# Performance work log

Measured on AMD Instinct MI355X. Metric: run time of the kernel, lower is better.

The kernel has to match this reference:

```python
import jax, jax.numpy as jnp
import numpy as np

B, D_IN = 8192, 4096
H1, H2, LAT = 2048, 1024, 256
NQ, NL = 16, 2


def setup_inputs() -> dict:
    key = jax.random.key(0)
    ks = jax.random.split(key, 16)
    def lin(k, fan_in, fan_out):
        k1, k2 = jax.random.split(k)
        s = 1.0 / np.sqrt(fan_in)
        W = jax.random.uniform(k1, (fan_out, fan_in), jnp.float32, -s, s)
        b = jax.random.uniform(k2, (fan_out,), jnp.float32, -s, s)
        return W, b
    x = jax.random.normal(ks[0], (B, D_IN), jnp.float32)
    We1, be1 = lin(ks[1], D_IN, H1)
    We2, be2 = lin(ks[2], H1, H2)
    We3, be3 = lin(ks[3], H2, LAT)
    P = jax.random.normal(ks[4], (NL, NQ, 3), jnp.float32)  # ansatz params (rx,ry,rz)
    Wd1, bd1 = lin(ks[5], NQ, H2)
    Wd2, bd2 = lin(ks[6], H2, H1)
    Wd3, bd3 = lin(ks[7], H1, D_IN)
    return {"x": x, "We1": We1, "be1": be1, "We2": We2, "be2": be2,
            "We3": We3, "be3": be3, "P": P, "Wd1": Wd1, "bd1": bd1,
            "Wd2": Wd2, "bd2": bd2, "Wd3": Wd3, "bd3": bd3}


def _quantum_block(latent, P):
    """Exact simulation of the per-qubit circuit (all gates single-qubit, so the
    2^n statevector factorizes into per-qubit 2-vectors (a,b) over |0>,|1>).
    latent: (B, LAT), P: (NL, NQ, 3). Returns Z-expectations (B, NQ)."""
    nq = P.shape[1]
    th = latent[:, :nq]  # encoding RY angles, (B, NQ)
    # RY(th)|0> = cos(th/2)|0> + sin(th/2)|1>
    a = jnp.cos(th / 2).astype(jnp.complex64)  # (B, NQ)
    b = jnp.sin(th / 2).astype(jnp.complex64)
    for l in range(P.shape[0]):
        # RX
        t = P[l, :, 0] / 2
        c, s = jnp.cos(t).astype(jnp.complex64), jnp.sin(t).astype(jnp.complex64)
        a, b = c * a - 1j * s * b, -1j * s * a + c * b
        # RY
        t = P[l, :, 1] / 2
        c, s = jnp.cos(t).astype(jnp.complex64), jnp.sin(t).astype(jnp.complex64)
        a, b = c * a - s * b, s * a + c * b
        # RZ
        t = P[l, :, 2] / 2
        ph = jnp.exp(-1j * t.astype(jnp.complex64))
        a, b = a * ph, b * jnp.conj(ph)
    z = (a.real ** 2 + a.imag ** 2) - (b.real ** 2 + b.imag ** 2)
    return z.astype(latent.dtype)


def reference(x, We1, be1, We2, be2, We3, be3, P,
              Wd1, bd1, Wd2, bd2, Wd3, bd3):
    h = jax.nn.relu(x @ We1.T + be1)
    h = jax.nn.relu(h @ We2.T + be2)
    latent = h @ We3.T + be3            # (B, LAT)
    refined = _quantum_block(latent, P)  # (B, NQ)
    h = jax.nn.relu(refined @ Wd1.T + bd1)
    h = jax.nn.relu(h @ Wd2.T + bd2)
    return h @ Wd3.T + bd3              # (B, D_IN)
```

## Files before the change

kernel.cpp:

```cpp
#include <hip/hip_runtime.h>

typedef __attribute__((ext_vector_type(8))) short bf16x8;
typedef __attribute__((ext_vector_type(16))) float f32x16;

__device__ __forceinline__ unsigned short f2bf(float f) {
    union { float f; unsigned int u; } v; v.f = f;
    unsigned int u = v.u;
    unsigned int r = (u + 0x7FFFu + ((u >> 16) & 1u)) >> 16;
    return (unsigned short)r;
}
__device__ __forceinline__ float bf2f(unsigned short b) {
    union { unsigned int u; float f; } v; v.u = ((unsigned int)b) << 16;
    return v.f;
}

#define GL16(g, l)                                                             \
    __builtin_amdgcn_global_load_lds(                                          \
        (__attribute__((address_space(1))) void*)(void*)(g),                   \
        (__attribute__((address_space(3))) void*)(void*)(l), 16, 0, 0)

#define BAR()   __builtin_amdgcn_s_barrier()
#define LGKM0() asm volatile("s_waitcnt lgkmcnt(0)" ::: "memory")

struct Cast5 {
    const float *s0, *s1, *s2, *s3, *s4;
    unsigned short *d0, *d1, *d2, *d3, *d4;
    int n0, n1, n2, n3, total;
};
__global__ void castall(Cast5 a) {
    int stride = gridDim.x * blockDim.x;
    for (int i = blockIdx.x * blockDim.x + threadIdx.x; i < a.total; i += stride) {
        int j = i; const float* s; unsigned short* d;
        if (j < a.n0) { s = a.s0; d = a.d0; }
        else { j -= a.n0;
            if (j < a.n1) { s = a.s1; d = a.d1; }
            else { j -= a.n1;
                if (j < a.n2) { s = a.s2; d = a.d2; }
                else { j -= a.n2;
                    if (j < a.n3) { s = a.s3; d = a.d3; }
                    else { j -= a.n3; s = a.s4; d = a.d4; } } } }
        float4 v = ((const float4*)s)[j];
        ushort4 o;
        o.x = f2bf(v.x); o.y = f2bf(v.y); o.z = f2bf(v.z); o.w = f2bf(v.w);
        ((ushort4*)d)[j] = o;
    }
}


template<int RELU, int OUT_BF16, int MP>
__global__ __launch_bounds__(512, 2) void gemm8p(
    const unsigned short* __restrict__ A,
    const unsigned short* __restrict__ Bm,
    const float* __restrict__ bias,
    void* __restrict__ Cout,
    int N, int K, int NT)
{
    constexpr int RT   = MP / 2;
    constexpr int AHU  = MP * 2048;
    constexpr int BOFF = MP * 8192;
    __shared__ __align__(16) unsigned short lds[MP * 8192 + 32768];

    const int tid  = threadIdx.x;
    const int lane = tid & 63;
    const int w    = tid >> 6;
    const int wm   = w >> 2;
    const int wn   = w & 3;
    const int bm   = blockIdx.y;
    const int bn   = blockIdx.x;

    const unsigned short* gA = A  + (long)bm * (MP * 64) * K;
    const unsigned short* gB = Bm + (long)bn * 256 * K;

    const int sr0 = tid >> 3;
    const int so0 = (((tid & 7) * 16) ^ ((sr0 & 7) << 4)) >> 1;
    const int loff = (sr0 * K + so0) * 2;
    const int ch1  = K * 128;
    const int lb0 = (w * 64) * 8;
    const int lb1 = (512 + w * 64) * 8;

    const int l31  = lane & 31;
    const int hi16 = (lane >> 5) * 16;
    const int aRow = wm * (MP * 16) + l31;
    const int bRow = wn * 32 + l31;
    const int swA  = (aRow & 7) << 4;
    const int swB  = (bRow & 7) << 4;
    int aK[4], bK[4];
    #pragma unroll
    for (int ks = 0; ks < 4; ++ks) {
        aK[ks] = aRow * 128 + ((ks * 32 + hi16) ^ swA);
        bK[ks] = MP * 16384 + bRow * 128 + ((ks * 32 + hi16) ^ swB);
    }

    f32x16 acc[2][2][RT] = {};
    bf16x8 a0[RT][4], a1[RT][4], b0[4], b1[4];

#define GLA_(SP, DI) do {                                                      \
        GL16((const char*)(SP) + loff, &lds[0] + (DI) + lb0);                  \
        if constexpr (MP == 4) {                                               \
            GL16((const char*)(SP) + loff + ch1, &lds[0] + (DI) + lb1); }      \
    } while (0)
#define GLB_(SP, DI) do {                                                      \
        GL16((const char*)(SP) + loff, &lds[0] + (DI) + lb0);                  \
        GL16((const char*)(SP) + loff + ch1, &lds[0] + (DI) + lb1);            \
    } while (0)

#define READA_(AR, MH, PAR) do {                                               \
        _Pragma("unroll") for (int rt_ = 0; rt_ < RT; ++rt_)                   \
        _Pragma("unroll") for (int ks_ = 0; ks_ < 4; ++ks_)                    \
            AR[rt_][ks_] = *(const bf16x8*)((const char*)lds + aK[ks_] +       \
                           (((PAR)*2+(MH))*MP*4096 + rt_*4096));               \
    } while (0)
#define READB_(BR, NH, PAR) do {                                               \
        _Pragma("unroll") for (int ks_ = 0; ks_ < 4; ++ks_)                    \
            BR[ks_] = *(const bf16x8*)((const char*)lds + bK[ks_] +            \
                      (((PAR)*2+(NH))*16384));                                 \
    } while (0)
#define QUAD(mh, nh, AR, BR) do {                                              \
        __builtin_amdgcn_s_setprio(1);                                         \
        _Pragma("unroll") for (int ks_ = 0; ks_ < 4; ++ks_)                    \
        _Pragma("unroll") for (int rt_ = 0; rt_ < RT; ++rt_)                   \
            acc[mh][nh][rt_] = __builtin_amdgcn_mfma_f32_32x32x16_bf16(        \
                AR[rt_][ks_], BR[ks_], acc[mh][nh][rt_], 0, 0, 0);             \
        __builtin_amdgcn_s_setprio(0);                                         \
    } while (0)
#define VMW() do {                                                             \
        if constexpr (MP == 4) asm volatile("s_waitcnt vmcnt(6)" ::: "memory");\
        else                   asm volatile("s_waitcnt vmcnt(5)" ::: "memory");\
    } while (0)

    GLB_(gB,                      BOFF + 0);
    GLA_(gA,                      0);
    GLB_(gB + (long)128 * K,      BOFF + 8192);
    GLA_(gA + (long)(MP*32) * K,  AHU);
    GLB_(gB + 64,                 BOFF + 2*8192);
    GLA_(gA + 64,                 2*AHU);
    GLB_(gB + (long)128 * K + 64, BOFF + 3*8192);
    VMW();
    BAR();
    READA_(a0, 0, 0);
    READB_(b0, 0, 0);

    const unsigned short* sA1 = gA + (long)(MP*32) * K + 64;
    const unsigned short* sA0 = gA + 128;
    const unsigned short* sB0 = gB + 128;
    const unsigned short* sB1 = gB + (long)128 * K + 128;

#define KTILE(T, PAR) do {                                                     \
        const int adv1_ = ((T) + 2 < NT) ? 64 : 0;                             \
        const int adv2_ = ((T) + 3 < NT) ? 64 : 0;                             \
                                                                       \
        READA_(a1, 1, PAR);                                                    \
        GLA_(sA1, (((PAR)^1)*2+1)*AHU); sA1 += adv1_;                          \
        BAR();                                                                 \
        QUAD(0, 0, a0, b0);                                                    \
                                                                       \
        READB_(b1, 1, PAR);                                                    \
        GLB_(sB0, BOFF + (PAR)*2*8192); sB0 += adv2_;                          \
        VMW();                                                                 \
        BAR();                                                                 \
        QUAD(0, 1, a0, b1);                                                    \
                                                                       \
        READA_(a0, 0, (PAR)^1);                                                \
        GLA_(sA0, (PAR)*2*AHU); sA0 += adv2_;                                  \
        BAR();                                                                 \
        QUAD(1, 1, a1, b1);                                                    \
                                                                       \
        GLB_(sB1, BOFF + ((PAR)*2+1)*8192); sB1 += adv2_;                      \
        VMW();                                                                 \
        BAR();                                                                 \
        QUAD(1, 0, a1, b0);                                                    \
        READB_(b0, 0, (PAR)^1);                                                \
    } while (0)

    for (int t = 0; t < NT; t += 2) {
        KTILE(t, 0);
        KTILE(t + 1, 1);
    }

    asm volatile("s_waitcnt vmcnt(0)" ::: "memory");
    BAR();

    const int rbase = (lane >> 5) * 4;
    float bv[2];
    #pragma unroll
    for (int nh = 0; nh < 2; ++nh)
        bv[nh] = bias[(long)bn * 256 + nh * 128 + wn * 32 + l31];

    if (OUT_BF16) {
        unsigned short* epi = lds;
        #pragma unroll
        for (int h = 0; h < 2; ++h) {
            if (h) { LGKM0(); BAR(); }
            #pragma unroll
            for (int rt = 0; rt < RT; ++rt)
                #pragma unroll
                for (int nh = 0; nh < 2; ++nh) {
                    int lcol = nh * 128 + wn * 32 + l31;
                    #pragma unroll
                    for (int reg = 0; reg < 16; ++reg) {
                        float v = acc[h][nh][rt][reg] + bv[nh];
                        if (RELU) v = fmaxf(v, 0.f);
                        int lrow = wm * (MP * 16) + rt * 32 +
                                   (reg & 3) + ((reg >> 2) << 3) + rbase;
                        epi[lrow * 264 + lcol] = f2bf(v);
                    }
                }
            LGKM0();
            BAR();
            long rowg0 = (long)bm * (MP * 64) + h * (MP * 32);
            #pragma unroll
            for (int i = 0; i < 2 * MP; ++i) {
                int row = (tid >> 5) + i * 16;
                int cc  = (tid & 31) * 8;
                bf16x8 v8 = *(const bf16x8*)&epi[row * 264 + cc];
                *(bf16x8*)((unsigned short*)Cout + (rowg0 + row) * (long)N + (long)bn * 256 + cc) = v8;
            }
        }
    } else {
        #pragma unroll
        for (int mh = 0; mh < 2; ++mh)
            #pragma unroll
            for (int rt = 0; rt < RT; ++rt)
                #pragma unroll
                for (int nh = 0; nh < 2; ++nh) {
                    long gcol = (long)bn * 256 + nh * 128 + wn * 32 + l31;
                    long growb = (long)bm * (MP * 64) + mh * (MP * 32) +
                                 wm * (MP * 16) + rt * 32 + rbase;
                    #pragma unroll
                    for (int reg = 0; reg < 16; ++reg) {
                        float v = acc[mh][nh][rt][reg] + bv[nh];
                        if (RELU) v = fmaxf(v, 0.f);
                        long grow = growb + (reg & 3) + ((reg >> 2) << 3);
                        ((float*)Cout)[grow * (long)N + gcol] = v;
                    }
                }
    }
#undef GLA_
#undef GLB_
#undef READA_
#undef READB_
#undef QUAD
#undef VMW
#undef KTILE
}

__global__ __launch_bounds__(256) void latq_d1(
    const unsigned short* __restrict__ h2,
    const float* __restrict__ We3,
    const float* __restrict__ be3,
    const float* __restrict__ P,
    const float* __restrict__ Wd1,
    const float* __restrict__ bd1,
    unsigned short* __restrict__ h3)
{
    __shared__ float zsh[4][16];
    const int lane = threadIdx.x & 63;
    const int wv   = threadIdx.x >> 6;
    const long row = (long)blockIdx.x * 4 + wv;

    float hreg[16];
    const unsigned short* hr = h2 + row * 1024;
    #pragma unroll
    for (int j = 0; j < 16; ++j) hreg[j] = bf2f(hr[lane + 64 * j]);

    float myth = 0.f;
    #pragma unroll
    for (int q = 0; q < 16; ++q) {
        const float* wq = We3 + q * 1024;
        float p = 0.f;
        #pragma unroll
        for (int j = 0; j < 16; ++j) p += hreg[j] * wq[lane + 64 * j];
        #pragma unroll
        for (int o = 32; o; o >>= 1) p += __shfl_xor(p, o, 64);
        if (lane == q) myth = p + be3[q];
    }

    if (lane < 16) {
        const int q = lane;
        float ar = cosf(0.5f * myth), ai = 0.f;
        float br = sinf(0.5f * myth), bi = 0.f;
        #pragma unroll
        for (int l = 0; l < 2; ++l) {
            const float* pp = P + (l * 16 + q) * 3;
            float t, c, s, ar2, ai2, br2, bi2;
            t = 0.5f * pp[0]; c = cosf(t); s = sinf(t);
            ar2 = c * ar + s * bi;  ai2 = c * ai - s * br;
            br2 = c * br + s * ai;  bi2 = c * bi - s * ar;
            ar = ar2; ai = ai2; br = br2; bi = bi2;
            t = 0.5f * pp[1]; c = cosf(t); s = sinf(t);
            ar2 = c * ar - s * br;  ai2 = c * ai - s * bi;
            br2 = s * ar + c * br;  bi2 = s * ai + c * bi;
            ar = ar2; ai = ai2; br = br2; bi = bi2;
            t = 0.5f * pp[2]; c = cosf(t); s = sinf(t);
            ar2 = ar * c + ai * s;  ai2 = ai * c - ar * s;
            br2 = br * c - bi * s;  bi2 = bi * c + br * s;
            ar = ar2; ai = ai2; br = br2; bi = bi2;
        }
        zsh[wv][q] = ar * ar + ai * ai - (br * br + bi * bi);
    }
    __syncthreads();

    float z[16];
    #pragma unroll
    for (int q = 0; q < 16; ++q) z[q] = zsh[wv][q];

    unsigned short* orow = h3 + row * 1024;
    #pragma unroll
    for (int i = 0; i < 16; ++i) {
        int j = lane + 64 * i;
        const float4* wrow = (const float4*)(Wd1 + j * 16);
        float acc = bd1[j];
        #pragma unroll
        for (int qq = 0; qq < 4; ++qq) {
            float4 w4 = wrow[qq];
            acc += z[qq * 4 + 0] * w4.x + z[qq * 4 + 1] * w4.y
                 + z[qq * 4 + 2] * w4.z + z[qq * 4 + 3] * w4.w;
        }
        orow[j] = f2bf(fmaxf(acc, 0.f));
    }
}

extern "C" void kernel_launch(void* const* d_in, const int* in_sizes, int n_in,
                              void* d_out, int out_size, void* d_ws, size_t ws_size,
                              hipStream_t stream) {
    const float* x   = (const float*)d_in[0];
    const float* We1 = (const float*)d_in[1];
    const float* be1 = (const float*)d_in[2];
    const float* We2 = (const float*)d_in[3];
    const float* be2 = (const float*)d_in[4];
    const float* We3 = (const float*)d_in[5];
    const float* be3 = (const float*)d_in[6];
    const float* P   = (const float*)d_in[7];
    const float* Wd1 = (const float*)d_in[8];
    const float* bd1 = (const float*)d_in[9];
    const float* Wd2 = (const float*)d_in[10];
    const float* bd2 = (const float*)d_in[11];
    const float* Wd3 = (const float*)d_in[12];
    const float* bd3 = (const float*)d_in[13];

    const int B = 8192, DIN = 4096, NH1 = 2048, NH2 = 1024;

    char* w = (char*)d_ws;
    unsigned short* x_bf   = (unsigned short*)(w);
    unsigned short* h4     = x_bf;
    unsigned short* We1_bf = (unsigned short*)(w + 67108864L);
    unsigned short* We2_bf = (unsigned short*)(w + 83886080L);
    unsigned short* Wd2_bf = (unsigned short*)(w + 88080384L);
    unsigned short* Wd3_bf = (unsigned short*)(w + 92274688L);
    unsigned short* h1     = (unsigned short*)(w + 109051904L);
    unsigned short* h3     = h1;
    unsigned short* h2     = (unsigned short*)(w + 142606336L);

    Cast5 ca;
    ca.s0 = x;   ca.d0 = x_bf;   ca.n0 = (int)((long)B * DIN / 4);
    ca.s1 = We1; ca.d1 = We1_bf; ca.n1 = (int)((long)NH1 * DIN / 4);
    ca.s2 = We2; ca.d2 = We2_bf; ca.n2 = (int)((long)NH2 * NH1 / 4);
    ca.s3 = Wd2; ca.d3 = Wd2_bf; ca.n3 = (int)((long)NH1 * NH2 / 4);
    ca.s4 = Wd3; ca.d4 = Wd3_bf;
    ca.total = ca.n0 + ca.n1 + ca.n2 + ca.n3 + (int)((long)DIN * NH1 / 4);
    castall<<<2048, 256, 0, stream>>>(ca);

    gemm8p<1, 1, 4><<<dim3(NH1 / 256, B / 256), 512, 0, stream>>>(x_bf, We1_bf, be1, h1, NH1, DIN, DIN >> 6);
    gemm8p<1, 1, 2><<<dim3(NH2 / 256, B / 128), 512, 0, stream>>>(h1, We2_bf, be2, h2, NH2, NH1, NH1 >> 6);
    latq_d1<<<dim3(B / 4), 256, 0, stream>>>(h2, We3, be3, P, Wd1, bd1, h3);
    gemm8p<1, 1, 4><<<dim3(NH1 / 256, B / 256), 512, 0, stream>>>(h3, Wd2_bf, bd2, h4, NH1, NH2, NH2 >> 6);
    gemm8p<0, 0, 4><<<dim3(DIN / 256, B / 256), 512, 0, stream>>>(h4, Wd3_bf, bd3, d_out, DIN, NH1, NH1 >> 6);
}
```

Measured before the change: 440.2 us.

## Switch GEMM LDS tile layout from XOR-swizzled rows to k-chunk-major columns

Changes how A and B tiles are laid out in LDS. Global loads now map consecutive threads to consecutive rows of one 16-byte k-chunk, so each chunk lands contiguously in LDS instead of in XOR-swizzled 128-byte rows. MFMA operand reads then use simple linear offsets with no per-lane swizzle. The aim is to cut LDS bank conflicts and address arithmetic on the reads, at the cost of less coalesced global loads, since each thread now fetches 16 bytes from a different row.

```diff
diff --git a/kernel.cpp b/kernel.cpp
--- a/kernel.cpp
+++ b/kernel.cpp
@@ -56,9 +56,12 @@
     int N, int K, int NT)
 {
     constexpr int RT   = MP / 2;
-    constexpr int AHU  = MP * 2048;
-    constexpr int BOFF = MP * 8192;
+    constexpr int ARWS = MP * 32;
+    constexpr int ASH  = (MP == 4) ? 7 : 6;
+    constexpr int AHB  = MP * 4096;
+    constexpr int BOFFB = 4 * AHB;
     __shared__ __align__(16) unsigned short lds[MP * 8192 + 32768];
+    char* ldsc = (char*)lds;
 
     const int tid  = threadIdx.x;
     const int lane = tid & 63;
@@ -71,49 +74,38 @@
     const unsigned short* gA = A  + (long)bm * (MP * 64) * K;
     const unsigned short* gB = Bm + (long)bn * 256 * K;
 
-    const int sr0 = tid >> 3;
-    const int so0 = (((tid & 7) * 16) ^ ((sr0 & 7) << 4)) >> 1;
-    const int loff = (sr0 * K + so0) * 2;
-    const int ch1  = K * 128;
-    const int lb0 = (w * 64) * 8;
-    const int lb1 = (512 + w * 64) * 8;
+    const int loffA = (tid & (ARWS - 1)) * (K * 2) + (tid >> ASH) * 16;
+    const int loffB = (tid & 127) * (K * 2) + (tid >> 7) * 16;
+    const int lwb   = w * 1024;
 
     const int l31  = lane & 31;
-    const int hi16 = (lane >> 5) * 16;
-    const int aRow = wm * (MP * 16) + l31;
-    const int bRow = wn * 32 + l31;
-    const int swA  = (aRow & 7) << 4;
-    const int swB  = (bRow & 7) << 4;
-    int aK[4], bK[4];
-    #pragma unroll
-    for (int ks = 0; ks < 4; ++ks) {
-        aK[ks] = aRow * 128 + ((ks * 32 + hi16) ^ swA);
-        bK[ks] = MP * 16384 + bRow * 128 + ((ks * 32 + hi16) ^ swB);
-    }
+    const int hi   = lane >> 5;
+    const int aBase = wm * (MP * 256) + l31 * 16 + hi * (ARWS * 16);
+    const int bBase = BOFFB + wn * 512 + l31 * 16 + hi * 2048;
 
     f32x16 acc[2][2][RT] = {};
     bf16x8 a0[RT][4], a1[RT][4], b0[4], b1[4];
 
 #define GLA_(SP, DI) do {                                                      \
-        GL16((const char*)(SP) + loff, &lds[0] + (DI) + lb0);                  \
+        GL16((const char*)(SP) + loffA, ldsc + (DI) + lwb);                    \
         if constexpr (MP == 4) {                                               \
-            GL16((const char*)(SP) + loff + ch1, &lds[0] + (DI) + lb1); }      \
+            GL16((const char*)(SP) + loffA + 64, ldsc + (DI) + 8192 + lwb); }  \
     } while (0)
 #define GLB_(SP, DI) do {                                                      \
-        GL16((const char*)(SP) + loff, &lds[0] + (DI) + lb0);                  \
-        GL16((const char*)(SP) + loff + ch1, &lds[0] + (DI) + lb1);            \
+        GL16((const char*)(SP) + loffB, ldsc + (DI) + lwb);                    \
+        GL16((const char*)(SP) + loffB + 64, ldsc + (DI) + 8192 + lwb);        \
     } while (0)
 
 #define READA_(AR, MH, PAR) do {                                               \
         _Pragma("unroll") for (int rt_ = 0; rt_ < RT; ++rt_)                   \
         _Pragma("unroll") for (int ks_ = 0; ks_ < 4; ++ks_)                    \
-            AR[rt_][ks_] = *(const bf16x8*)((const char*)lds + aK[ks_] +       \
-                           (((PAR)*2+(MH))*MP*4096 + rt_*4096));               \
+            AR[rt_][ks_] = *(const bf16x8*)(ldsc + aBase +                     \
+                (((PAR)*2+(MH))*AHB + rt_*512 + ks_*(ARWS*32)));               \
     } while (0)
 #define READB_(BR, NH, PAR) do {                                               \
         _Pragma("unroll") for (int ks_ = 0; ks_ < 4; ++ks_)                    \
-            BR[ks_] = *(const bf16x8*)((const char*)lds + bK[ks_] +            \
-                      (((PAR)*2+(NH))*16384));                                 \
+            BR[ks_] = *(const bf16x8*)(ldsc + bBase +                          \
+                (((PAR)*2+(NH))*16384 + ks_*4096));                            \
     } while (0)
 #define QUAD(mh, nh, AR, BR) do {                                              \
         __builtin_amdgcn_s_setprio(1);                                         \
@@ -128,13 +120,13 @@
         else                   asm volatile("s_waitcnt vmcnt(5)" ::: "memory");\
     } while (0)
 
-    GLB_(gB,                      BOFF + 0);
+    GLB_(gB,                      BOFFB + 0);
     GLA_(gA,                      0);
-    GLB_(gB + (long)128 * K,      BOFF + 8192);
-    GLA_(gA + (long)(MP*32) * K,  AHU);
-    GLB_(gB + 64,                 BOFF + 2*8192);
-    GLA_(gA + 64,                 2*AHU);
-    GLB_(gB + (long)128 * K + 64, BOFF + 3*8192);
+    GLB_(gB + (long)128 * K,      BOFFB + 16384);
+    GLA_(gA + (long)(MP*32) * K,  AHB);
+    GLB_(gB + 64,                 BOFFB + 2*16384);
+    GLA_(gA + 64,                 2*AHB);
+    GLB_(gB + (long)128 * K + 64, BOFFB + 3*16384);
     VMW();
     BAR();
     READA_(a0, 0, 0);
@@ -150,22 +142,22 @@
         const int adv2_ = ((T) + 3 < NT) ? 64 : 0;                             \
                                                                        \
         READA_(a1, 1, PAR);                                                    \
-        GLA_(sA1, (((PAR)^1)*2+1)*AHU); sA1 += adv1_;                          \
+        GLA_(sA1, (((PAR)^1)*2+1)*AHB); sA1 += adv1_;                          \
         BAR();                                                                 \
         QUAD(0, 0, a0, b0);                                                    \
                                                                        \
         READB_(b1, 1, PAR);                                                    \
-        GLB_(sB0, BOFF + (PAR)*2*8192); sB0 += adv2_;                          \
+        GLB_(sB0, BOFFB + (PAR)*2*16384); sB0 += adv2_;                        \
         VMW();                                                                 \
         BAR();                                                                 \
         QUAD(0, 1, a0, b1);                                                    \
                                                                        \
         READA_(a0, 0, (PAR)^1);                                                \
-        GLA_(sA0, (PAR)*2*AHU); sA0 += adv2_;                                  \
+        GLA_(sA0, (PAR)*2*AHB); sA0 += adv2_;                                  \
         BAR();                                                                 \
         QUAD(1, 1, a1, b1);                                                    \
                                                                        \
-        GLB_(sB1, BOFF + ((PAR)*2+1)*8192); sB1 += adv2_;                      \
+        GLB_(sB1, BOFFB + ((PAR)*2+1)*16384); sB1 += adv2_;                    \
         VMW();                                                                 \
         BAR();                                                                 \
         QUAD(1, 0, a1, b0);                                                    \
@@ -180,7 +172,7 @@
     asm volatile("s_waitcnt vmcnt(0)" ::: "memory");
     BAR();
 
-    const int rbase = (lane >> 5) * 4;
+    const int rbase = hi * 4;
     float bv[2];
     #pragma unroll
     for (int nh = 0; nh < 2; ++nh)
```

New measurement: 503.0 us. 1.14x slower.
